# Kernel tuning notes

Measured on AMD Instinct MI355X. Metric: run time of the kernel, lower is better.

The kernel has to match this reference:

```python
import jax, jax.numpy as jnp
import numpy as np

B, S, D = 2, 2048, 2048
H, KVH, DH = 16, 4, 128
EPS = 1e-6
ROPE_BASE = 10000.0


def _rms_norm(x, eps=EPS):
    # weightless RMSNorm over the last (head) dim
    return x * jax.lax.rsqrt(jnp.mean(jnp.square(x), axis=-1, keepdims=True) + eps)


def _rope(x):
    # x: [b, s, h, d]; standard half-split RoPE, base 10000
    d = x.shape[-1]
    s = x.shape[1]
    inv_freq = 1.0 / (ROPE_BASE ** (jnp.arange(0, d // 2, dtype=jnp.float32) * 2.0 / d))
    ang = jnp.arange(s, dtype=jnp.float32)[:, None] * inv_freq[None, :]  # [s, d/2]
    cos = jnp.cos(ang)[None, :, None, :]
    sin = jnp.sin(ang)[None, :, None, :]
    x1, x2 = jnp.split(x, 2, axis=-1)
    return jnp.concatenate([x1 * cos - x2 * sin, x1 * sin + x2 * cos], axis=-1)


def setup_inputs() -> dict:
    key = jax.random.key(0)
    ks = jax.random.split(key, 5)
    x = jax.random.normal(ks[0], (B, S, D), dtype=jnp.float32)
    mask = jnp.tril(jnp.ones((S, S), dtype=bool))  # causal
    # eqx.Linear-style weights: [out, in], scaled init
    wq = jax.random.normal(ks[1], (D, D), dtype=jnp.float32) / np.sqrt(D)
    wk = jax.random.normal(ks[2], (KVH * DH, D), dtype=jnp.float32) / np.sqrt(D)
    wv = jax.random.normal(ks[3], (KVH * DH, D), dtype=jnp.float32) / np.sqrt(D)
    wo = jax.random.normal(ks[4], (D, D), dtype=jnp.float32) / np.sqrt(D)
    return {"x": x, "mask": mask, "wq": wq, "wk": wk, "wv": wv, "wo": wo}


def reference(x, mask, wq, wk, wv, wo):
    b, s, _ = x.shape
    q = jnp.einsum('bsi,oi->bso', x, wq).reshape(b, s, H, DH)
    k = jnp.einsum('bsi,oi->bso', x, wk).reshape(b, s, KVH, DH)
    v = jnp.einsum('bsi,oi->bso', x, wv).reshape(b, s, KVH, DH)
    rep = H // KVH
    k = jnp.repeat(k, rep, axis=-2)  # [b, s, H, DH]
    v = jnp.repeat(v, rep, axis=-2)
    q = _rms_norm(q)
    k = _rms_norm(k)
    q = _rope(q)
    k = _rope(k)
    scores = jnp.einsum('bshd,bthd->bhst', q, k) / jnp.sqrt(jnp.float32(DH))
    scores = jnp.where(mask[None, None], scores, -jnp.inf)
    w = jax.nn.softmax(scores, axis=-1)
    out = jnp.einsum('bhst,bthd->bshd', w, v).reshape(b, s, D)
    return jnp.einsum('bsi,oi->bso', out, wo)
```

## Files before the change

kernel.cpp:

```cpp
#include <hip/hip_runtime.h>
#include <hip/hip_bf16.h>

typedef unsigned short u16;
typedef unsigned int   u32;
typedef unsigned long long u64;
typedef __attribute__((ext_vector_type(8))) short bf16x8;
typedef __attribute__((ext_vector_type(4))) float f32x4;
typedef __attribute__((ext_vector_type(16))) float f32x16;

#define MFMA16(a,b,c) __builtin_amdgcn_mfma_f32_16x16x32_bf16((a),(b),(c),0,0,0)
#define MFMA32(a,b,c) __builtin_amdgcn_mfma_f32_32x32x16_bf16((a),(b),(c),0,0,0)

#define GLD16(gp, lp) __builtin_amdgcn_global_load_lds( \
    (const __attribute__((address_space(1))) void*)(gp), \
    (__attribute__((address_space(3))) void*)(lp), 16, 0, 0)

__device__ inline u32 pkbf(float a, float b) {
  __hip_bfloat16 ha = __float2bfloat16(a), hb = __float2bfloat16(b);
  return (u32)(*(u16*)&ha) | ((u32)(*(u16*)&hb) << 16);
}
__device__ inline float b2f(u16 x) {
  __hip_bfloat16 h; *(u16*)&h = x; return __bfloat162float(h);
}
__device__ inline u32 pk2(float a, float b) {
  u32 ua = __builtin_bit_cast(u32, a) + 0x8000u;
  u32 ub = __builtin_bit_cast(u32, b) + 0x8000u;
  return __builtin_amdgcn_perm(ub, ua, 0x07060302u);
}
__device__ inline float fmax3(float a, float b, float c) {
  return fmaxf(fmaxf(a, b), c);
}

__global__ __launch_bounds__(256) void cast_f32_bf16(const float* __restrict__ src,
                                                     u16* __restrict__ dst, int n4) {
  int i = blockIdx.x * 256 + threadIdx.x;
  if (i >= n4) return;
  float4 v = reinterpret_cast<const float4*>(src)[i];
  uint2 pk; pk.x = pkbf(v.x, v.y); pk.y = pkbf(v.z, v.w);
  reinterpret_cast<uint2*>(dst)[i] = pk;
}

__device__ inline void cstore(u16* C, size_t i, float v) {
  __hip_bfloat16 h = __float2bfloat16(v); C[i] = *(u16*)&h;
}
__device__ inline void cstore(float* C, size_t i, float v) { C[i] = v; }

template<typename OutT>
__global__ __launch_bounds__(256) void gemm_bt(const u16* __restrict__ A,
                                               const u16* __restrict__ B,
                                               OutT* __restrict__ C,
                                               int M, int N, int K) {
  __shared__ u16 As[128 * 32];
  __shared__ u16 Bs[128 * 32];
  const int t = threadIdx.x;
  const int lane = t & 63, wid = t >> 6;
  const int l15 = lane & 15, l4 = lane >> 4;
  const int wr = wid >> 1, wc = wid & 1;

  const int nwg = gridDim.x * gridDim.y;
  int lid = blockIdx.y * gridDim.x + blockIdx.x;
  lid = (lid & 7) * (nwg >> 3) + (lid >> 3);
  const int m0 = (lid / gridDim.x) * 128, n0 = (lid % gridDim.x) * 128;

  const int srow = t >> 2, scol = (t & 3) << 3;
  const u16* Ag = A + (size_t)(m0 + srow) * K + scol;
  const u16* Bg = B + (size_t)(n0 + srow) * K + scol;
  u16* As_d  = &As[srow * 32 + scol];
  u16* As_d2 = &As[(srow + 64) * 32 + scol];
  u16* Bs_d  = &Bs[srow * 32 + scol];
  u16* Bs_d2 = &Bs[(srow + 64) * 32 + scol];

  const int fra = wr * 64 + l15;
  const int frb = wc * 64 + l15;
  const int fk  = l4 << 3;

  f32x4 acc[4][4] = {};
  for (int k0 = 0; k0 < K; k0 += 32) {
    __syncthreads();
    GLD16(Ag + k0,                 As_d);
    GLD16(Ag + (size_t)64*K + k0,  As_d2);
    GLD16(Bg + k0,                 Bs_d);
    GLD16(Bg + (size_t)64*K + k0,  Bs_d2);
    __syncthreads();
    bf16x8 af[4], bfr[4];
#pragma unroll
    for (int m = 0; m < 4; ++m) af[m]  = *(const bf16x8*)&As[(fra + m*16)*32 + fk];
#pragma unroll
    for (int n = 0; n < 4; ++n) bfr[n] = *(const bf16x8*)&Bs[(frb + n*16)*32 + fk];
#pragma unroll
    for (int m = 0; m < 4; ++m)
#pragma unroll
      for (int n = 0; n < 4; ++n)
        acc[m][n] = MFMA16(af[m], bfr[n], acc[m][n]);
  }
  const int crow = m0 + wr * 64 + (l4 << 2);
  const int ccol = n0 + wc * 64 + l15;
#pragma unroll
  for (int m = 0; m < 4; ++m)
#pragma unroll
    for (int n = 0; n < 4; ++n)
#pragma unroll
      for (int r = 0; r < 4; ++r)
        cstore(C, (size_t)(crow + m*16 + r) * N + (ccol + n*16), acc[m][n][r]);
}

__global__ __launch_bounds__(256) void rmsrope_kernel(u16* __restrict__ qkv) {
  const int t = threadIdx.x;
  const int lane = t & 63;
  const int gw = blockIdx.x * 4 + (t >> 6);
  const int row = gw / 20;
  const int hd = gw - row * 20;
  const int col = (hd < 16) ? hd * 128 : 2048 + (hd - 16) * 128;
  const size_t base = (size_t)row * 3072 + col;
  float x1 = b2f(qkv[base + lane]);
  float x2 = b2f(qkv[base + 64 + lane]);
  float ss = x1 * x1 + x2 * x2;
#pragma unroll
  for (int off = 32; off >= 1; off >>= 1) ss += __shfl_xor(ss, off, 64);
  const float qsc = (hd < 16) ? (0.08838834764831845f * 1.44269504088896340f)
                              : 1.0f;
  const float sc = rsqrtf(ss * (1.0f / 128.0f) + 1e-6f) * qsc;
  const int pos = row & 2047;
  const float inv_freq = exp2f(-(float)lane * (13.287712379549449f / 64.0f));
  float sn, cs;
  sincosf((float)pos * inv_freq, &sn, &cs);
  const float a = x1 * sc, b2 = x2 * sc;
  __hip_bfloat16 o1 = __float2bfloat16(a * cs - b2 * sn);
  __hip_bfloat16 o2 = __float2bfloat16(a * sn + b2 * cs);
  qkv[base + lane] = *(u16*)&o1;
  qkv[base + 64 + lane] = *(u16*)&o2;
}

__global__ __launch_bounds__(256) void vtrans_kernel(const u16* __restrict__ qkv,
                                                     u16* __restrict__ vt) {
  __shared__ u16 Ls[64 * 130];
  const int t = threadIdx.x;
  const int g = blockIdx.x & 7, sb = blockIdx.x >> 3;
  const int b = g >> 2, kvh = g & 3;
  const int vcol = 2560 + kvh * 128;
  {
    const int row = t >> 4, dch = t & 15;
    const u16* src = qkv + (size_t)(b * 2048 + sb * 64 + row) * 3072 + vcol + dch * 8;
#pragma unroll
    for (int it = 0; it < 4; ++it) {
      bf16x8 v = *(const bf16x8*)(src + (size_t)it * 16 * 3072);
      *(bf16x8*)&Ls[(row + it * 16) * 130 + dch * 8] = v;
    }
  }
  __syncthreads();
  const int c = t & 7, d0 = t >> 3;
  const int k0 = 4 * (8 * (c >> 2) + 4 * ((c >> 1) & 1) + (c & 1));
#pragma unroll
  for (int it = 0; it < 4; ++it) {
    const int d = d0 + 32 * it;
    u16 v[8];
#pragma unroll
    for (int e = 0; e < 8; ++e)
      v[e] = Ls[(k0 + (e & 3) + 8 * (e >> 2)) * 130 + d];
    u64 lo = (u64)v[0] | ((u64)v[1] << 16) | ((u64)v[2] << 32) | ((u64)v[3] << 48);
    u64 hi = (u64)v[4] | ((u64)v[5] << 16) | ((u64)v[6] << 32) | ((u64)v[7] << 48);
    u64* dst = (u64*)(vt + ((size_t)g * 128 + d) * 2048 + sb * 64 + c * 8);
    dst[0] = lo; dst[1] = hi;
  }
}

__global__ __launch_bounds__(256, 2) void attn_kernel(const u16* __restrict__ qkv,
                                                      const u16* __restrict__ vt,
                                                      u16* __restrict__ ao) {
  __shared__ u16 Ks[2][64 * 128];
  __shared__ u16 Vt[2][128 * 64];

  const int t = threadIdx.x;
  const int lane = t & 63, w = t >> 6;
  const int l31 = lane & 31, hi = lane >> 5;
  const int qg = w >> 1, hi2 = w & 1;

  const int bid = blockIdx.x;
  const int g = bid & 7;
  const int b = g >> 2, kvh = g & 3;
  const int idx = bid >> 3;
  const int h = kvh * 4 + (idx & 3);
  const int j = idx >> 2;

  const int kcol = 2048 + kvh * 128;
  const u16* vtg = vt + (size_t)g * 128 * 2048;

  const int krow_s = t >> 4, kchk = t & 15;
  const int vd = t >> 3, vc = t & 7;

#define STAGE_K(kb_, buf_) do {                                               \
    const size_t rb_ = (size_t)(b * 2048 + (kb_) * 64);                       \
    _Pragma("unroll")                                                         \
    for (int j_ = 0; j_ < 4; ++j_) {                                          \
      const int row_ = j_ * 16 + krow_s;                                      \
      GLD16(qkv + (rb_ + row_) * 3072 + kcol + ((kchk ^ (row_ & 7)) << 3),    \
            &Ks[buf_][(j_ * 256 + t) << 3]);                                  \
    } } while (0)

#define STAGE_V(kb_, buf_) do {                                               \
    _Pragma("unroll")                                                         \
    for (int j_ = 0; j_ < 4; ++j_) {                                          \
      const int d_ = j_ * 32 + vd;                                            \
      GLD16(vtg + (size_t)d_ * 2048 + (kb_) * 64 + ((vc ^ (d_ & 7)) << 3),    \
            &Vt[buf_][(j_ * 256 + t) << 3]);                                  \
    } } while (0)

  for (int ph = 0; ph < 2; ++ph) {
    const int qt64 = ph ? (31 - j) : j;
    const int q0 = qt64 * 64;
    const int nt = qt64 + 1;
    const int qrow = q0 + 32 * qg + l31;

    bf16x8 qf[8];
    {
      const u16* qp = qkv + (size_t)(b * 2048 + qrow) * 3072 + h * 128 + hi * 8;
#pragma unroll
      for (int st = 0; st < 8; ++st) qf[st] = *(const bf16x8*)(qp + st * 16);
    }

    f32x16 o[4];
#pragma unroll
    for (int dt = 0; dt < 4; ++dt)
#pragma unroll
      for (int i = 0; i < 16; ++i) o[dt][i] = 0.f;
    float m2 = -1e30f, l = 0.f;

    STAGE_K(0, 0);
    STAGE_V(0, 0);

    for (int kb = 0; kb < nt; ++kb) {
      const int cur = kb & 1;
      __syncthreads();
      const bool have_next = (kb + 1 < nt);
      if (have_next) {
        STAGE_K(kb + 1, cur ^ 1);
        STAGE_V(kb + 1, cur ^ 1);
      }

      f32x16 s;
#pragma unroll
      for (int i = 0; i < 16; ++i) s[i] = 0.f;
      const int kbase = (32 * hi2 + l31) * 128;
      const int ksw = l31 & 7;
      __builtin_amdgcn_s_setprio(1);
#pragma unroll
      for (int st = 0; st < 8; ++st) {
        bf16x8 ka = *(const bf16x8*)&Ks[cur][kbase + (((2 * st + hi) ^ ksw) << 3)];
        s = MFMA32(ka, qf[st], s);
      }
      __builtin_amdgcn_s_setprio(0);

      const bool nomask = (kb < qt64) || (hi2 == 0 && qg == 1);
      if (!nomask) {
#pragma unroll
        for (int i = 0; i < 16; ++i) {
          const int kr = kb * 64 + 32 * hi2 + (i & 3) + 8 * (i >> 2) + 4 * hi;
          s[i] = (kr <= qrow) ? s[i] : -INFINITY;
        }
      }
      float a0 = fmax3(s[0], s[1], s[2]);
      float a1 = fmax3(s[3], s[4], s[5]);
      float a2 = fmax3(s[6], s[7], s[8]);
      float a3 = fmax3(s[9], s[10], s[11]);
      float a4 = fmax3(s[12], s[13], s[14]);
      float b0 = fmax3(a0, a1, s[15]);
      float b1 = fmax3(a2, a3, a4);
      float pm = fmaxf(b0, b1);
      pm = fmaxf(pm, __shfl_xor(pm, 32));
      if (!__all(pm <= m2 + 8.f)) {
        const float m2n = fmaxf(m2, pm);
        const float fc = exp2f(m2 - m2n);
        m2 = m2n; l *= fc;
#pragma unroll
        for (int dt = 0; dt < 4; ++dt)
#pragma unroll
          for (int i = 0; i < 16; ++i) o[dt][i] *= fc;
      }
#pragma unroll
      for (int i = 0; i < 16; ++i) s[i] = exp2f(s[i] - m2);
      float t8[8];
#pragma unroll
      for (int i = 0; i < 8; ++i) t8[i] = s[i] + s[i + 8];
#pragma unroll
      for (int i = 0; i < 4; ++i) t8[i] = t8[i] + t8[i + 4];
      l += (t8[0] + t8[1]) + (t8[2] + t8[3]);
      union PB { u32 wd[4]; bf16x8 v; } p0u, p1u;
#pragma unroll
      for (int q_ = 0; q_ < 4; ++q_) {
        p0u.wd[q_] = pk2(s[2 * q_],     s[2 * q_ + 1]);
        p1u.wd[q_] = pk2(s[8 + 2 * q_], s[8 + 2 * q_ + 1]);
      }
      __builtin_amdgcn_s_setprio(1);
#pragma unroll
      for (int dt = 0; dt < 4; ++dt) {
        const int vrow = (dt * 32 + l31) * 64;
        const int dsw = l31 & 7;
        bf16x8 va0 = *(const bf16x8*)&Vt[cur][vrow + (((4 * hi2 + hi) ^ dsw) << 3)];
        o[dt] = MFMA32(va0, p0u.v, o[dt]);
        bf16x8 va1 = *(const bf16x8*)&Vt[cur][vrow + (((4 * hi2 + 2 + hi) ^ dsw) << 3)];
        o[dt] = MFMA32(va1, p1u.v, o[dt]);
      }
      __builtin_amdgcn_s_setprio(0);
    }

    __syncthreads();
    const float l_tot = l + __shfl_xor(l, 32);
    float* Mrg = (float*)&Ks[0][0];
    float* Mlb = (float*)&Vt[0][0];
    const int sw8 = l31 & 7;
    if (hi2) {
#pragma unroll
      for (int dt = 0; dt < 4; ++dt) {
        const int rbase = ((qg * 4 + dt) * 32 + l31) * 32;
#pragma unroll
        for (int m_ = 0; m_ < 4; ++m_) {
          f32x4 cv;
          cv[0] = o[dt][4 * m_ + 0]; cv[1] = o[dt][4 * m_ + 1];
          cv[2] = o[dt][4 * m_ + 2]; cv[3] = o[dt][4 * m_ + 3];
          *(f32x4*)&Mrg[rbase + (((hi * 4 + m_) ^ sw8) << 2)] = cv;
        }
      }
      if (hi == 0) {
        Mlb[qg * 64 + l31] = m2;
        Mlb[qg * 64 + 32 + l31] = l_tot;
      }
    }
    __syncthreads();
    if (!hi2) {
      const float m1 = Mlb[qg * 64 + l31];
      const float l1 = Mlb[qg * 64 + 32 + l31];
      const float ms = fmaxf(m2, m1);
      const float w0 = exp2f(m2 - ms), w1 = exp2f(m1 - ms);
      const float inv = 1.f / (w0 * l_tot + w1 * l1);
      const float aw0 = w0 * inv, aw1 = w1 * inv;
      const size_t orow = (size_t)(b * 2048 + qrow) * 2048 + h * 128;
#pragma unroll
      for (int dt = 0; dt < 4; ++dt) {
        const int rbase = ((qg * 4 + dt) * 32 + l31) * 32;
#pragma unroll
        for (int m_ = 0; m_ < 4; ++m_) {
          f32x4 o1v = *(const f32x4*)&Mrg[rbase + (((hi * 4 + m_) ^ sw8) << 2)];
          u64 val = 0;
#pragma unroll
          for (int r = 0; r < 4; ++r) {
            __hip_bfloat16 hb =
                __float2bfloat16(aw0 * o[dt][4 * m_ + r] + aw1 * o1v[r]);
            val |= (u64)(*(u16*)&hb) << (16 * r);
          }
          *(u64*)&ao[orow + dt * 32 + 8 * m_ + 4 * hi] = val;
        }
      }
    }
    __syncthreads();
  }
#undef STAGE_K
#undef STAGE_V
}

extern "C" void kernel_launch(void* const* d_in, const int* in_sizes, int n_in,
                              void* d_out, int out_size, void* d_ws, size_t ws_size,
                              hipStream_t stream) {
  const float* x  = (const float*)d_in[0];
  const float* wq = (const float*)d_in[2];
  const float* wk = (const float*)d_in[3];
  const float* wv = (const float*)d_in[4];
  const float* wo = (const float*)d_in[5];
  float* out = (float*)d_out;

  u16* xb   = (u16*)d_ws;
  u16* wqkv = xb + (size_t)8388608;
  u16* qkv  = wqkv + (size_t)6291456;
  u16* vtg  = qkv + (size_t)12582912;
  u16* ao   = xb;
  u16* wob  = wqkv;

  cast_f32_bf16<<<8192, 256, 0, stream>>>(x,  xb,   2097152);
  cast_f32_bf16<<<4096, 256, 0, stream>>>(wq, wqkv, 1048576);
  cast_f32_bf16<<<1024, 256, 0, stream>>>(wk, wqkv + (size_t)4194304, 262144);
  cast_f32_bf16<<<1024, 256, 0, stream>>>(wv, wqkv + (size_t)5242880, 262144);

  gemm_bt<u16><<<dim3(24, 32), 256, 0, stream>>>(xb, wqkv, qkv, 4096, 3072, 2048);

  cast_f32_bf16<<<4096, 256, 0, stream>>>(wo, wob, 1048576);

  rmsrope_kernel<<<20480, 256, 0, stream>>>(qkv);
  vtrans_kernel<<<256, 256, 0, stream>>>(qkv, vtg);

  attn_kernel<<<512, 256, 0, stream>>>(qkv, vtg, ao);

  gemm_bt<float><<<dim3(16, 32), 256, 0, stream>>>(ao, wob, out, 4096, 2048, 2048);
}
```

Baseline: 234.2 us.

## Rewrite GEMM with 128x256 tiles, double-buffered LDS prefetch and swizzle

```diff
diff --git a/kernel.cpp b/kernel.cpp
--- a/kernel.cpp
+++ b/kernel.cpp
@@ -46,62 +46,80 @@
 __device__ inline void cstore(float* C, size_t i, float v) { C[i] = v; }
 
 template<typename OutT>
-__global__ __launch_bounds__(256) void gemm_bt(const u16* __restrict__ A,
-                                               const u16* __restrict__ B,
-                                               OutT* __restrict__ C,
-                                               int M, int N, int K) {
-  __shared__ u16 As[128 * 32];
-  __shared__ u16 Bs[128 * 32];
+__global__ __launch_bounds__(512, 4) void gemm_big(const u16* __restrict__ A,
+                                                   const u16* __restrict__ B,
+                                                   OutT* __restrict__ C,
+                                                   int M, int N, int K) {
+  __shared__ u16 As[2][128 * 32];
+  __shared__ u16 Bs[2][256 * 32];
+
   const int t = threadIdx.x;
   const int lane = t & 63, wid = t >> 6;
   const int l15 = lane & 15, l4 = lane >> 4;
-  const int wr = wid >> 1, wc = wid & 1;
+  const int wr = wid >> 2, wc = wid & 3;
 
   const int nwg = gridDim.x * gridDim.y;
   int lid = blockIdx.y * gridDim.x + blockIdx.x;
   lid = (lid & 7) * (nwg >> 3) + (lid >> 3);
-  const int m0 = (lid / gridDim.x) * 128, n0 = (lid % gridDim.x) * 128;
-
-  const int srow = t >> 2, scol = (t & 3) << 3;
-  const u16* Ag = A + (size_t)(m0 + srow) * K + scol;
-  const u16* Bg = B + (size_t)(n0 + srow) * K + scol;
-  u16* As_d  = &As[srow * 32 + scol];
-  u16* As_d2 = &As[(srow + 64) * 32 + scol];
-  u16* Bs_d  = &Bs[srow * 32 + scol];
-  u16* Bs_d2 = &Bs[(srow + 64) * 32 + scol];
-
-  const int fra = wr * 64 + l15;
-  const int frb = wc * 64 + l15;
-  const int fk  = l4 << 3;
+  const int m0 = (lid / gridDim.x) * 128, n0 = (lid % gridDim.x) * 256;
+
+  const int ra = t >> 2;
+  const int ca = (t & 3) ^ ((ra >> 1) & 3);
+  const u16* Ag  = A + (size_t)(m0 + ra) * K + ca * 8;
+  const u16* Bg0 = B + (size_t)(n0 + ra) * K + ca * 8;
+  const u16* Bg1 = B + (size_t)(n0 + 128 + ra) * K + ca * 8;
+
+#define STAGE(k0_, buf_) do {                                                 \
+    GLD16(Ag  + (k0_), &As[buf_][t * 8]);                                     \
+    GLD16(Bg0 + (k0_), &Bs[buf_][t * 8]);                                     \
+    GLD16(Bg1 + (k0_), &Bs[buf_][4096 + t * 8]);                              \
+  } while (0)
+
+  const int nk = K >> 5;
+  const int ks = (l15 >> 1) & 3;
+  const int coff = ((l4 ^ ks) << 3);
 
   f32x4 acc[4][4] = {};
-  for (int k0 = 0; k0 < K; k0 += 32) {
-    __syncthreads();
-    GLD16(Ag + k0,                 As_d);
-    GLD16(Ag + (size_t)64*K + k0,  As_d2);
-    GLD16(Bg + k0,                 Bs_d);
-    GLD16(Bg + (size_t)64*K + k0,  Bs_d2);
-    __syncthreads();
+
+  STAGE(0, 0);
+  STAGE(32, 1);
+
+  for (int j = 0; j < nk; ++j) {
+    const int cur = j & 1;
+    if (j + 1 < nk) asm volatile("s_waitcnt vmcnt(3)" ::: "memory");
+    else            asm volatile("s_waitcnt vmcnt(0)" ::: "memory");
+    __builtin_amdgcn_s_barrier();
+    __builtin_amdgcn_sched_barrier(0);
+
     bf16x8 af[4], bfr[4];
 #pragma unroll
-    for (int m = 0; m < 4; ++m) af[m]  = *(const bf16x8*)&As[(fra + m*16)*32 + fk];
-#pragma unroll
-    for (int n = 0; n < 4; ++n) bfr[n] = *(const bf16x8*)&Bs[(frb + n*16)*32 + fk];
-#pragma unroll
-    for (int m = 0; m < 4; ++m)
-#pragma unroll
-      for (int n = 0; n < 4; ++n)
-        acc[m][n] = MFMA16(af[m], bfr[n], acc[m][n]);
+    for (int mi = 0; mi < 4; ++mi)
+      af[mi] = *(const bf16x8*)&As[cur][(wr * 64 + mi * 16 + l15) * 32 + coff];
+#pragma unroll
+    for (int ni = 0; ni < 4; ++ni)
+      bfr[ni] = *(const bf16x8*)&Bs[cur][(wc * 64 + ni * 16 + l15) * 32 + coff];
+    __builtin_amdgcn_s_setprio(1);
+#pragma unroll
+    for (int mi = 0; mi < 4; ++mi)
+#pragma unroll
+      for (int ni = 0; ni < 4; ++ni)
+        acc[mi][ni] = MFMA16(af[mi], bfr[ni], acc[mi][ni]);
+    __builtin_amdgcn_s_setprio(0);
+
+    __builtin_amdgcn_s_barrier();
+    if (j + 2 < nk) STAGE((j + 2) << 5, cur);
   }
+
   const int crow = m0 + wr * 64 + (l4 << 2);
   const int ccol = n0 + wc * 64 + l15;
 #pragma unroll
-  for (int m = 0; m < 4; ++m)
-#pragma unroll
-    for (int n = 0; n < 4; ++n)
+  for (int mi = 0; mi < 4; ++mi)
+#pragma unroll
+    for (int ni = 0; ni < 4; ++ni)
 #pragma unroll
       for (int r = 0; r < 4; ++r)
-        cstore(C, (size_t)(crow + m*16 + r) * N + (ccol + n*16), acc[m][n][r]);
+        cstore(C, (size_t)(crow + mi * 16 + r) * N + (ccol + ni * 16), acc[mi][ni][r]);
+#undef STAGE
 }
 
 __global__ __launch_bounds__(256) void rmsrope_kernel(u16* __restrict__ qkv) {
@@ -379,7 +397,7 @@
   cast_f32_bf16<<<1024, 256, 0, stream>>>(wk, wqkv + (size_t)4194304, 262144);
   cast_f32_bf16<<<1024, 256, 0, stream>>>(wv, wqkv + (size_t)5242880, 262144);
 
-  gemm_bt<u16><<<dim3(24, 32), 256, 0, stream>>>(xb, wqkv, qkv, 4096, 3072, 2048);
+  gemm_big<u16><<<dim3(12, 32), 512, 0, stream>>>(xb, wqkv, qkv, 4096, 3072, 2048);
 
   cast_f32_bf16<<<4096, 256, 0, stream>>>(wo, wob, 1048576);
 
@@ -388,5 +406,5 @@
 
   attn_kernel<<<512, 256, 0, stream>>>(qkv, vtg, ao);
 
-  gemm_bt<float><<<dim3(16, 32), 256, 0, stream>>>(ao, wob, out, 4096, 2048, 2048);
-}
+  gemm_big<float><<<dim3(8, 32), 512, 0, stream>>>(ao, wob, out, 4096, 2048, 2048);
+}
```

Result: faster. 219.8 us (-6.1%).
